# Kernel tuning notes

Measured on AMD Instinct MI355X. Metric: run time of the kernel, lower is better.

The kernel has to match this reference:

```python
import jax, jax.numpy as jnp
import numpy as np

N_NODES = 10000
N_EDGES = 320000
T = 24
H = 64


def setup_inputs() -> dict:
    key = jax.random.key(0)
    ks = jax.random.split(key, 16)
    s = 0.1  # keep LSTM gates in a sane range
    return {
        "blob": jax.random.normal(ks[0], (N_NODES, T), dtype=jnp.float32),
        "W_ih": s * jax.random.normal(ks[1], (N_NODES, 4 * H, 1), dtype=jnp.float32),
        "b_ih": s * jax.random.normal(ks[2], (N_NODES, 4 * H), dtype=jnp.float32),
        "W_hh": s * jax.random.normal(ks[3], (N_NODES, 4 * H, H), dtype=jnp.float32),
        "b_hh": s * jax.random.normal(ks[4], (N_NODES, 4 * H), dtype=jnp.float32),
        "Wg0": s * jax.random.normal(ks[5], (H, H), dtype=jnp.float32),
        "bg0": s * jax.random.normal(ks[6], (H,), dtype=jnp.float32),
        "Wg1": s * jax.random.normal(ks[7], (H, H), dtype=jnp.float32),
        "bg1": s * jax.random.normal(ks[8], (H,), dtype=jnp.float32),
        "Wg2": s * jax.random.normal(ks[9], (H, 1), dtype=jnp.float32),
        "bg2": s * jax.random.normal(ks[10], (1,), dtype=jnp.float32),
        "edge_src": jax.random.randint(ks[11], (N_EDGES,), 0, N_NODES, dtype=jnp.int32),
        "edge_dst": jax.random.randint(ks[12], (N_EDGES,), 0, N_NODES, dtype=jnp.int32),
    }


def _sym_norms(edge_src, edge_dst, n, dtype):
    ones = jnp.ones(edge_src.shape[0], dtype=dtype)
    deg_out = jax.ops.segment_sum(ones, edge_src, num_segments=n)
    deg_in = jax.ops.segment_sum(ones, edge_dst, num_segments=n)
    inv_sqrt = lambda d: jnp.where(d > 0, jnp.where(d > 0, d, 1.0) ** -0.5, 0.0)
    return inv_sqrt(deg_out), inv_sqrt(deg_in)


def reference(blob, W_ih, b_ih, W_hh, b_hh, Wg0, bg0, Wg1, bg1, Wg2, bg2,
              edge_src, edge_dst):
    n = blob.shape[0]
    norm_src, norm_dst = _sym_norms(edge_src, edge_dst, n, blob.dtype)

    def gconv(h, W, b, act=None):
        # DGL GraphConv, norm='both': D_dst^{-1/2} A D_src^{-1/2} h W + b
        msg = (h * norm_src[:, None])[edge_src]            # [E, F]
        agg = jax.ops.segment_sum(msg, edge_dst, num_segments=n)
        out = (agg * norm_dst[:, None]) @ W + b
        return act(out) if act is not None else out

    # Per-node LSTM, batched across all nodes; torch gate order i,f,g,o.
    Wx = W_ih[:, :, 0]  # [N, 4H] since in_feats == 1

    def step(carry, x_t):
        h, c = carry  # [N,H] each
        gates = (Wx * x_t[:, None] + b_ih
                 + jnp.einsum('nh,ngh->ng', h, W_hh) + b_hh)  # [N,4H]
        i, f, g, o = jnp.split(gates, 4, axis=1)
        c = jax.nn.sigmoid(f) * c + jax.nn.sigmoid(i) * jnp.tanh(g)
        h = jax.nn.sigmoid(o) * jnp.tanh(c)
        # GCN stack on current hidden states (dropout is identity at eval)
        z = gconv(h, Wg0, bg0, jax.nn.relu)
        z = gconv(z, Wg1, bg1, jax.nn.relu)
        z = gconv(z, Wg2, bg2)                               # [N,1]
        return (h, c), z[:, 0]

    h0 = jnp.zeros((n, H), dtype=blob.dtype)
    c0 = jnp.zeros((n, H), dtype=blob.dtype)
    _, ys = jax.lax.scan(step, (h0, c0), blob.T)  # ys: [T, N]
    return ys.T  # [N, T]
```

## Files before the change

### kernel.cpp

```cpp
#include <hip/hip_runtime.h>
#include <hip/hip_fp16.h>
#include <cstdint>
#include <cstddef>

#define NN 10000
#define NE 320000
#define TT 24
#define TP 12
#define HD 64
#define G4 256

__device__ __forceinline__ float sigm(float x){ return 1.0f/(1.0f + __expf(-x)); }
__device__ __forceinline__ float tanh_fast(float x){ return 2.0f/(1.0f + __expf(-2.0f*x)) - 1.0f; }

__global__ __launch_bounds__(256) void degree_kernel(const int* __restrict__ esrc, const int* __restrict__ edst,
                                                     int* __restrict__ deg_out, int* __restrict__ deg_in){
  int e = blockIdx.x*256 + threadIdx.x;
  if (e < NE){
    atomicAdd(&deg_out[esrc[e]], 1);
    atomicAdd(&deg_in[edst[e]], 1);
  }
}

__global__ __launch_bounds__(256) void norm_kernel(const int* __restrict__ deg_out, const int* __restrict__ deg_in,
                                                   float* __restrict__ norm_src, float* __restrict__ norm_dst){
  int i = blockIdx.x*256 + threadIdx.x;
  if (i < NN){
    int a = deg_out[i]; norm_src[i] = (a>0) ? rsqrtf((float)a) : 0.0f;
    int b = deg_in[i];  norm_dst[i] = (b>0) ? rsqrtf((float)b) : 0.0f;
  }
}

__global__ __launch_bounds__(256) void scan_kernel(const int* __restrict__ deg_in, int* __restrict__ csr_off,
                                                   int* __restrict__ cursor){
  __shared__ int sums[256];
  const int CH = (NN + 255)/256;
  int tid = threadIdx.x;
  int beg = tid*CH; if (beg > NN) beg = NN;
  int end = beg+CH; if (end > NN) end = NN;
  int s = 0;
  for (int i=beg;i<end;i++) s += deg_in[i];
  sums[tid] = s;
  __syncthreads();
  if (tid == 0){
    int run = 0;
    for (int i=0;i<256;i++){ int v = sums[i]; sums[i] = run; run += v; }
  }
  __syncthreads();
  int run = sums[tid];
  for (int i=beg;i<end;i++){ csr_off[i] = run; cursor[i] = run; run += deg_in[i]; }
  if (tid == 0) csr_off[NN] = NE;
}

__global__ __launch_bounds__(256) void fill_kernel(const int* __restrict__ esrc, const int* __restrict__ edst,
                                                   int* __restrict__ cursor, int2* __restrict__ csr_pk,
                                                   const float* __restrict__ norm_src){
  int e = blockIdx.x*256 + threadIdx.x;
  if (e < NE){
    int d = edst[e]; int s = esrc[e];
    int pos = atomicAdd(&cursor[d], 1);
    csr_pk[pos] = make_int2(s, __float_as_int(norm_src[s]));
  }
}

__global__ __launch_bounds__(256) void lstm_kernel(const float* __restrict__ blob, const float* __restrict__ W_ih,
                                                   const float* __restrict__ b_ih, const float* __restrict__ W_hh,
                                                   const float* __restrict__ b_hh, __half* __restrict__ h_all){
  const int n = blockIdx.x;
  const int g = threadIdx.x;
  __shared__ float lh[HD];
  __shared__ float lg[G4];

  float4 w4[16];
  const float4* wp = reinterpret_cast<const float4*>(W_hh + (size_t)n*(G4*HD) + (size_t)g*HD);
  #pragma unroll
  for (int i=0;i<16;i++) w4[i] = wp[i];

  const float wx = W_ih[(size_t)n*G4 + g];
  const float bs = b_ih[(size_t)n*G4 + g] + b_hh[(size_t)n*G4 + g];

  float c = 0.0f;
  if (g < HD) lh[g] = 0.0f;
  __syncthreads();

  for (int t=0;t<TT;t++){
    float xt = blob[n*TT + t];
    float gate = fmaf(wx, xt, bs);
    const float4* h4 = reinterpret_cast<const float4*>(lh);
    #pragma unroll
    for (int i=0;i<16;i++){
      float4 hv = h4[i];
      gate = fmaf(hv.x, w4[i].x, gate);
      gate = fmaf(hv.y, w4[i].y, gate);
      gate = fmaf(hv.z, w4[i].z, gate);
      gate = fmaf(hv.w, w4[i].w, gate);
    }
    lg[g] = gate;
    __syncthreads();
    if (g < HD){
      float iv = sigm(lg[g]);
      float fv = sigm(lg[HD+g]);
      float gv = tanh_fast(lg[2*HD+g]);
      float ov = sigm(lg[3*HD+g]);
      c = fmaf(fv, c, iv*gv);
      float h = ov * tanh_fast(c);
      lh[g] = h;
      h_all[(((size_t)n*TP + (t>>1))*HD + g)*2 + (t&1)] = __float2half(h);
    }
    __syncthreads();
  }
}

__global__ __launch_bounds__(256) void gconv_mid_kernel(const __half2* __restrict__ src_feat, __half2* __restrict__ dst_feat,
                                                        const float* __restrict__ Wg, const float* __restrict__ bg,
                                                        const int* __restrict__ csr_off, const int2* __restrict__ csr_pk,
                                                        const float* __restrict__ norm_dst){
  int wid = blockIdx.x*4 + (threadIdx.x >> 6);
  int lane = threadIdx.x & 63;
  if (wid >= NN*2) return;
  int n  = wid >> 1;
  int hf = wid & 1;
  const int tpo = hf*6;

  float wcol[HD];
  #pragma unroll
  for (int k=0;k<HD;k++) wcol[k] = Wg[k*HD + lane];
  float bias = bg[lane];

  float2 acc[6];
  #pragma unroll
  for (int j=0;j<6;j++) acc[j] = make_float2(0.f, 0.f);

  int e = csr_off[n];
  const int end = csr_off[n+1];
  for (; e+1 < end; e += 2){
    int2 p0 = csr_pk[e];
    int2 p1 = csr_pk[e+1];
    float w0 = __int_as_float(p0.y);
    float w1 = __int_as_float(p1.y);
    const __half2* b0 = src_feat + (size_t)p0.x*(TP*HD) + tpo*HD + lane;
    const __half2* b1 = src_feat + (size_t)p1.x*(TP*HD) + tpo*HD + lane;
    __half2 u0[6], u1[6];
    #pragma unroll
    for (int j=0;j<6;j++) u0[j] = b0[j*HD];
    #pragma unroll
    for (int j=0;j<6;j++) u1[j] = b1[j*HD];
    #pragma unroll
    for (int j=0;j<6;j++){
      float2 f0 = __half22float2(u0[j]);
      float2 f1 = __half22float2(u1[j]);
      acc[j].x = fmaf(w0, f0.x, acc[j].x);
      acc[j].y = fmaf(w0, f0.y, acc[j].y);
      acc[j].x = fmaf(w1, f1.x, acc[j].x);
      acc[j].y = fmaf(w1, f1.y, acc[j].y);
    }
  }
  if (e < end){
    int2 p0 = csr_pk[e];
    float w0 = __int_as_float(p0.y);
    const __half2* b0 = src_feat + (size_t)p0.x*(TP*HD) + tpo*HD + lane;
    #pragma unroll
    for (int j=0;j<6;j++){
      float2 f0 = __half22float2(b0[j*HD]);
      acc[j].x = fmaf(w0, f0.x, acc[j].x);
      acc[j].y = fmaf(w0, f0.y, acc[j].y);
    }
  }
  float nd = norm_dst[n];
  #pragma unroll
  for (int j=0;j<6;j++){ acc[j].x *= nd; acc[j].y *= nd; }

  __half2* dbase = dst_feat + (size_t)n*(TP*HD) + tpo*HD + lane;
  #pragma unroll
  for (int j=0;j<6;j++){
    float oe = bias, oo = bias;
    #pragma unroll
    for (int k=0;k<HD;k++){
      float ae = __shfl(acc[j].x, k, 64);
      float ao = __shfl(acc[j].y, k, 64);
      oe = fmaf(ae, wcol[k], oe);
      oo = fmaf(ao, wcol[k], oo);
    }
    oe = fmaxf(oe, 0.0f);
    oo = fmaxf(oo, 0.0f);
    dbase[j*HD] = __floats2half2_rn(oe, oo);
  }
}

__global__ __launch_bounds__(256) void gconv_last_kernel(const __half2* __restrict__ src_feat, float* __restrict__ q,
                                                         const float* __restrict__ Wg, const float* __restrict__ bg,
                                                         const float* __restrict__ Wg2,
                                                         const int* __restrict__ csr_off, const int2* __restrict__ csr_pk,
                                                         const float* __restrict__ norm_dst, const float* __restrict__ norm_src){
  int wid = blockIdx.x*4 + (threadIdx.x >> 6);
  int lane = threadIdx.x & 63;
  if (wid >= NN*2) return;
  int n  = wid >> 1;
  int hf = wid & 1;
  const int tpo = hf*6;

  float wcol[HD];
  #pragma unroll
  for (int k=0;k<HD;k++) wcol[k] = Wg[k*HD + lane];
  float bias = bg[lane];
  float w2 = Wg2[lane];

  float2 acc[6];
  #pragma unroll
  for (int j=0;j<6;j++) acc[j] = make_float2(0.f, 0.f);

  int e = csr_off[n];
  const int end = csr_off[n+1];
  for (; e+1 < end; e += 2){
    int2 p0 = csr_pk[e];
    int2 p1 = csr_pk[e+1];
    float w0 = __int_as_float(p0.y);
    float w1 = __int_as_float(p1.y);
    const __half2* b0 = src_feat + (size_t)p0.x*(TP*HD) + tpo*HD + lane;
    const __half2* b1 = src_feat + (size_t)p1.x*(TP*HD) + tpo*HD + lane;
    __half2 u0[6], u1[6];
    #pragma unroll
    for (int j=0;j<6;j++) u0[j] = b0[j*HD];
    #pragma unroll
    for (int j=0;j<6;j++) u1[j] = b1[j*HD];
    #pragma unroll
    for (int j=0;j<6;j++){
      float2 f0 = __half22float2(u0[j]);
      float2 f1 = __half22float2(u1[j]);
      acc[j].x = fmaf(w0, f0.x, acc[j].x);
      acc[j].y = fmaf(w0, f0.y, acc[j].y);
      acc[j].x = fmaf(w1, f1.x, acc[j].x);
      acc[j].y = fmaf(w1, f1.y, acc[j].y);
    }
  }
  if (e < end){
    int2 p0 = csr_pk[e];
    float w0 = __int_as_float(p0.y);
    const __half2* b0 = src_feat + (size_t)p0.x*(TP*HD) + tpo*HD + lane;
    #pragma unroll
    for (int j=0;j<6;j++){
      float2 f0 = __half22float2(b0[j*HD]);
      acc[j].x = fmaf(w0, f0.x, acc[j].x);
      acc[j].y = fmaf(w0, f0.y, acc[j].y);
    }
  }
  float nd = norm_dst[n];
  #pragma unroll
  for (int j=0;j<6;j++){ acc[j].x *= nd; acc[j].y *= nd; }

  float ns = norm_src[n];
  #pragma unroll
  for (int j=0;j<6;j++){
    float oe = bias, oo = bias;
    #pragma unroll
    for (int k=0;k<HD;k++){
      float ae = __shfl(acc[j].x, k, 64);
      float ao = __shfl(acc[j].y, k, 64);
      oe = fmaf(ae, wcol[k], oe);
      oo = fmaf(ao, wcol[k], oo);
    }
    oe = fmaxf(oe, 0.0f) * w2;
    oo = fmaxf(oo, 0.0f) * w2;
    #pragma unroll
    for (int off=32; off; off >>= 1){
      oe += __shfl_xor(oe, off, 64);
      oo += __shfl_xor(oo, off, 64);
    }
    if (lane == 0){
      int tp = tpo + j;
      q[n*32 + 2*tp]     = oe * ns;
      q[n*32 + 2*tp + 1] = oo * ns;
    }
  }
}

__global__ __launch_bounds__(256) void out_kernel(const float* __restrict__ q, const int* __restrict__ csr_off,
                                                  const int2* __restrict__ csr_pk, const float* __restrict__ norm_dst,
                                                  const float* __restrict__ bg2, float* __restrict__ out){
  int n = blockIdx.x*4 + (threadIdx.x >> 6);
  int lane = threadIdx.x & 63;
  if (n >= NN) return;
  int sub = lane >> 5;
  int tl  = lane & 31;
  bool act = tl < TT;
  int e = csr_off[n];
  const int end = csr_off[n+1];
  float s0 = 0.f, s1 = 0.f;
  for (; e+3 < end; e += 4){
    int a = csr_pk[e+sub].x;
    int b = csr_pk[e+2+sub].x;
    if (act){
      s0 += q[a*32 + tl];
      s1 += q[b*32 + tl];
    }
  }
  for (; e+1 < end; e += 2){
    int a = csr_pk[e+sub].x;
    if (act) s0 += q[a*32 + tl];
  }
  if (e < end && sub == 0 && act) s1 += q[csr_pk[e].x*32 + tl];
  float s = s0 + s1;
  s += __shfl_xor(s, 32, 64);
  if (sub == 0 && act) out[n*TT + tl] = fmaf(norm_dst[n], s, bg2[0]);
}

extern "C" void kernel_launch(void* const* d_in, const int* in_sizes, int n_in,
                              void* d_out, int out_size, void* d_ws, size_t ws_size,
                              hipStream_t stream) {
  (void)in_sizes; (void)n_in; (void)out_size; (void)ws_size;
  const float* blob  = (const float*)d_in[0];
  const float* W_ih  = (const float*)d_in[1];
  const float* b_ih  = (const float*)d_in[2];
  const float* W_hh  = (const float*)d_in[3];
  const float* b_hh  = (const float*)d_in[4];
  const float* Wg0   = (const float*)d_in[5];
  const float* bg0   = (const float*)d_in[6];
  const float* Wg1   = (const float*)d_in[7];
  const float* bg1   = (const float*)d_in[8];
  const float* Wg2   = (const float*)d_in[9];
  const float* bg2   = (const float*)d_in[10];
  const int* edge_src = (const int*)d_in[11];
  const int* edge_dst = (const int*)d_in[12];
  float* out = (float*)d_out;

  char* ws = (char*)d_ws;
  size_t off = 0;
  auto alloc = [&](size_t bytes)->char* {
    char* p = ws + off; off += (bytes + 255) & ~(size_t)255; return p;
  };
  __half* h_all   = (__half*)alloc((size_t)NN*TT*HD*sizeof(__half));
  __half* z1      = (__half*)alloc((size_t)NN*TT*HD*sizeof(__half));
  float*  q       = (float*) alloc((size_t)NN*32*sizeof(float));
  int*    deg_out = (int*)   alloc((size_t)NN*sizeof(int));
  int*    deg_in  = (int*)   alloc((size_t)NN*sizeof(int));
  float*  norm_src= (float*) alloc((size_t)NN*sizeof(float));
  float*  norm_dst= (float*) alloc((size_t)NN*sizeof(float));
  int*    csr_off = (int*)   alloc((size_t)(NN+1)*sizeof(int));
  int*    cursor  = (int*)   alloc((size_t)NN*sizeof(int));
  int2*   csr_pk  = (int2*)  alloc((size_t)NE*sizeof(int2));

  hipMemsetAsync(deg_out, 0, (size_t)NN*sizeof(int), stream);
  hipMemsetAsync(deg_in,  0, (size_t)NN*sizeof(int), stream);

  degree_kernel<<<(NE+255)/256, 256, 0, stream>>>(edge_src, edge_dst, deg_out, deg_in);
  norm_kernel<<<(NN+255)/256, 256, 0, stream>>>(deg_out, deg_in, norm_src, norm_dst);
  scan_kernel<<<1, 256, 0, stream>>>(deg_in, csr_off, cursor);
  fill_kernel<<<(NE+255)/256, 256, 0, stream>>>(edge_src, edge_dst, cursor, csr_pk, norm_src);

  lstm_kernel<<<NN, 256, 0, stream>>>(blob, W_ih, b_ih, W_hh, b_hh, h_all);

  gconv_mid_kernel<<<(NN*2+3)/4, 256, 0, stream>>>((const __half2*)h_all, (__half2*)z1, Wg0, bg0,
                                                   csr_off, csr_pk, norm_dst);
  gconv_last_kernel<<<(NN*2+3)/4, 256, 0, stream>>>((const __half2*)z1, q, Wg1, bg1, Wg2,
                                                    csr_off, csr_pk, norm_dst, norm_src);
  out_kernel<<<(NN+3)/4, 256, 0, stream>>>(q, csr_off, csr_pk, norm_dst, bg2, out);
}
```

Baseline: 1.406 ms.

## Store per-lane contiguous time features and stream GCN weights instead of register-caching

Changes the hidden-state layout so each feature lane's 12 half2 timestep pairs are contiguous per half, allowing 8-byte vector gathers per edge instead of six strided 4-byte loads. The LSTM buffers h in registers and writes it once at the end. The GCN kernels drop the 64-register weight column cache, load Wg per k inside a loop interchanged over time slots, and add an occupancy hint of 8 blocks. This aims to cut gather transactions and register pressure, at the cost of repeated weight loads from cache.

```diff
diff --git a/kernel.cpp b/kernel.cpp
--- a/kernel.cpp
+++ b/kernel.cpp
@@ -6,12 +6,21 @@
 #define NN 10000
 #define NE 320000
 #define TT 24
-#define TP 12
 #define HD 64
 #define G4 256
+#define NODE_HALFS (2*HD*12)
 
 __device__ __forceinline__ float sigm(float x){ return 1.0f/(1.0f + __expf(-x)); }
 __device__ __forceinline__ float tanh_fast(float x){ return 2.0f/(1.0f + __expf(-2.0f*x)) - 1.0f; }
+
+__device__ __forceinline__ float2 h2f2(unsigned int u){
+  __half2 h = *reinterpret_cast<const __half2*>(&u);
+  return __half22float2(h);
+}
+__device__ __forceinline__ unsigned int f2h2(float a, float b){
+  __half2 h = __floats2half2_rn(a, b);
+  return *reinterpret_cast<unsigned int*>(&h);
+}
 
 __global__ __launch_bounds__(256) void degree_kernel(const int* __restrict__ esrc, const int* __restrict__ edst,
                                                      int* __restrict__ deg_out, int* __restrict__ deg_in){
@@ -80,9 +89,12 @@
   const float bs = b_ih[(size_t)n*G4 + g] + b_hh[(size_t)n*G4 + g];
 
   float c = 0.0f;
+  float hprev = 0.0f;
+  unsigned int hb[12];
   if (g < HD) lh[g] = 0.0f;
   __syncthreads();
 
+  #pragma unroll
   for (int t=0;t<TT;t++){
     float xt = blob[n*TT + t];
     float gate = fmaf(wx, xt, bs);
@@ -105,13 +117,25 @@
       c = fmaf(fv, c, iv*gv);
       float h = ov * tanh_fast(c);
       lh[g] = h;
-      h_all[(((size_t)n*TP + (t>>1))*HD + g)*2 + (t&1)] = __float2half(h);
+      if (t & 1) hb[t>>1] = f2h2(hprev, h);
+      else       hprev = h;
     }
     __syncthreads();
   }
-}
-
-__global__ __launch_bounds__(256) void gconv_mid_kernel(const __half2* __restrict__ src_feat, __half2* __restrict__ dst_feat,
+  if (g < HD){
+    #pragma unroll
+    for (int hf=0; hf<2; hf++){
+      uint2* dst = reinterpret_cast<uint2*>(h_all + ((size_t)(n*2+hf)*HD + g)*12);
+      #pragma unroll
+      for (int m=0; m<3; m++){
+        uint2 s; s.x = hb[hf*6 + 2*m]; s.y = hb[hf*6 + 2*m + 1];
+        dst[m] = s;
+      }
+    }
+  }
+}
+
+__global__ __launch_bounds__(256, 8) void gconv_mid_kernel(const __half* __restrict__ src_feat, __half* __restrict__ dst_feat,
                                                         const float* __restrict__ Wg, const float* __restrict__ bg,
                                                         const int* __restrict__ csr_off, const int2* __restrict__ csr_pk,
                                                         const float* __restrict__ norm_dst){
@@ -120,12 +144,7 @@
   if (wid >= NN*2) return;
   int n  = wid >> 1;
   int hf = wid & 1;
-  const int tpo = hf*6;
-
-  float wcol[HD];
-  #pragma unroll
-  for (int k=0;k<HD;k++) wcol[k] = Wg[k*HD + lane];
-  float bias = bg[lane];
+  const size_t lane_off = ((size_t)hf*HD + lane)*12;
 
   float2 acc[6];
   #pragma unroll
@@ -138,56 +157,71 @@
     int2 p1 = csr_pk[e+1];
     float w0 = __int_as_float(p0.y);
     float w1 = __int_as_float(p1.y);
-    const __half2* b0 = src_feat + (size_t)p0.x*(TP*HD) + tpo*HD + lane;
-    const __half2* b1 = src_feat + (size_t)p1.x*(TP*HD) + tpo*HD + lane;
-    __half2 u0[6], u1[6];
-    #pragma unroll
-    for (int j=0;j<6;j++) u0[j] = b0[j*HD];
-    #pragma unroll
-    for (int j=0;j<6;j++) u1[j] = b1[j*HD];
-    #pragma unroll
-    for (int j=0;j<6;j++){
-      float2 f0 = __half22float2(u0[j]);
-      float2 f1 = __half22float2(u1[j]);
-      acc[j].x = fmaf(w0, f0.x, acc[j].x);
-      acc[j].y = fmaf(w0, f0.y, acc[j].y);
-      acc[j].x = fmaf(w1, f1.x, acc[j].x);
-      acc[j].y = fmaf(w1, f1.y, acc[j].y);
+    const uint2* b0 = reinterpret_cast<const uint2*>(src_feat + (size_t)p0.x*NODE_HALFS + lane_off);
+    const uint2* b1 = reinterpret_cast<const uint2*>(src_feat + (size_t)p1.x*NODE_HALFS + lane_off);
+    uint2 u0[3], u1[3];
+    #pragma unroll
+    for (int m=0;m<3;m++) u0[m] = b0[m];
+    #pragma unroll
+    for (int m=0;m<3;m++) u1[m] = b1[m];
+    #pragma unroll
+    for (int m=0;m<3;m++){
+      float2 f0a = h2f2(u0[m].x), f0b = h2f2(u0[m].y);
+      float2 f1a = h2f2(u1[m].x), f1b = h2f2(u1[m].y);
+      acc[2*m].x   = fmaf(w0, f0a.x, acc[2*m].x);
+      acc[2*m].y   = fmaf(w0, f0a.y, acc[2*m].y);
+      acc[2*m+1].x = fmaf(w0, f0b.x, acc[2*m+1].x);
+      acc[2*m+1].y = fmaf(w0, f0b.y, acc[2*m+1].y);
+      acc[2*m].x   = fmaf(w1, f1a.x, acc[2*m].x);
+      acc[2*m].y   = fmaf(w1, f1a.y, acc[2*m].y);
+      acc[2*m+1].x = fmaf(w1, f1b.x, acc[2*m+1].x);
+      acc[2*m+1].y = fmaf(w1, f1b.y, acc[2*m+1].y);
     }
   }
   if (e < end){
     int2 p0 = csr_pk[e];
     float w0 = __int_as_float(p0.y);
-    const __half2* b0 = src_feat + (size_t)p0.x*(TP*HD) + tpo*HD + lane;
+    const uint2* b0 = reinterpret_cast<const uint2*>(src_feat + (size_t)p0.x*NODE_HALFS + lane_off);
+    uint2 u0[3];
+    #pragma unroll
+    for (int m=0;m<3;m++) u0[m] = b0[m];
+    #pragma unroll
+    for (int m=0;m<3;m++){
+      float2 f0a = h2f2(u0[m].x), f0b = h2f2(u0[m].y);
+      acc[2*m].x   = fmaf(w0, f0a.x, acc[2*m].x);
+      acc[2*m].y   = fmaf(w0, f0a.y, acc[2*m].y);
+      acc[2*m+1].x = fmaf(w0, f0b.x, acc[2*m+1].x);
+      acc[2*m+1].y = fmaf(w0, f0b.y, acc[2*m+1].y);
+    }
+  }
+  float nd = norm_dst[n];
+  #pragma unroll
+  for (int j=0;j<6;j++){ acc[j].x *= nd; acc[j].y *= nd; }
+
+  float bias = bg[lane];
+  float oe[6], oo[6];
+  #pragma unroll
+  for (int j=0;j<6;j++){ oe[j] = bias; oo[j] = bias; }
+  #pragma unroll
+  for (int k=0;k<HD;k++){
+    float wk = Wg[k*HD + lane];
     #pragma unroll
     for (int j=0;j<6;j++){
-      float2 f0 = __half22float2(b0[j*HD]);
-      acc[j].x = fmaf(w0, f0.x, acc[j].x);
-      acc[j].y = fmaf(w0, f0.y, acc[j].y);
-    }
-  }
-  float nd = norm_dst[n];
-  #pragma unroll
-  for (int j=0;j<6;j++){ acc[j].x *= nd; acc[j].y *= nd; }
-
-  __half2* dbase = dst_feat + (size_t)n*(TP*HD) + tpo*HD + lane;
-  #pragma unroll
-  for (int j=0;j<6;j++){
-    float oe = bias, oo = bias;
-    #pragma unroll
-    for (int k=0;k<HD;k++){
-      float ae = __shfl(acc[j].x, k, 64);
-      float ao = __shfl(acc[j].y, k, 64);
-      oe = fmaf(ae, wcol[k], oe);
-      oo = fmaf(ao, wcol[k], oo);
-    }
-    oe = fmaxf(oe, 0.0f);
-    oo = fmaxf(oo, 0.0f);
-    dbase[j*HD] = __floats2half2_rn(oe, oo);
-  }
-}
-
-__global__ __launch_bounds__(256) void gconv_last_kernel(const __half2* __restrict__ src_feat, float* __restrict__ q,
+      oe[j] = fmaf(__shfl(acc[j].x, k, 64), wk, oe[j]);
+      oo[j] = fmaf(__shfl(acc[j].y, k, 64), wk, oo[j]);
+    }
+  }
+  uint2* dst = reinterpret_cast<uint2*>(dst_feat + (size_t)n*NODE_HALFS + lane_off);
+  #pragma unroll
+  for (int m=0;m<3;m++){
+    uint2 s;
+    s.x = f2h2(fmaxf(oe[2*m],   0.0f), fmaxf(oo[2*m],   0.0f));
+    s.y = f2h2(fmaxf(oe[2*m+1], 0.0f), fmaxf(oo[2*m+1], 0.0f));
+    dst[m] = s;
+  }
+}
+
+__global__ __launch_bounds__(256, 8) void gconv_last_kernel(const __half* __restrict__ src_feat, float* __restrict__ q,
                                                          const float* __restrict__ Wg, const float* __restrict__ bg,
                                                          const float* __restrict__ Wg2,
                                                          const int* __restrict__ csr_off, const int2* __restrict__ csr_pk,
@@ -197,13 +231,7 @@
   if (wid >= NN*2) return;
   int n  = wid >> 1;
   int hf = wid & 1;
-  const int tpo = hf*6;
-
-  float wcol[HD];
-  #pragma unroll
-  for (int k=0;k<HD;k++) wcol[k] = Wg[k*HD + lane];
-  float bias = bg[lane];
-  float w2 = Wg2[lane];
+  const size_t lane_off = ((size_t)hf*HD + lane)*12;
 
   float2 acc[6];
   #pragma unroll
@@ -216,60 +244,74 @@
     int2 p1 = csr_pk[e+1];
     float w0 = __int_as_float(p0.y);
     float w1 = __int_as_float(p1.y);
-    const __half2* b0 = src_feat + (size_t)p0.x*(TP*HD) + tpo*HD + lane;
-    const __half2* b1 = src_feat + (size_t)p1.x*(TP*HD) + tpo*HD + lane;
-    __half2 u0[6], u1[6];
-    #pragma unroll
-    for (int j=0;j<6;j++) u0[j] = b0[j*HD];
-    #pragma unroll
-    for (int j=0;j<6;j++) u1[j] = b1[j*HD];
-    #pragma unroll
-    for (int j=0;j<6;j++){
-      float2 f0 = __half22float2(u0[j]);
-      float2 f1 = __half22float2(u1[j]);
-      acc[j].x = fmaf(w0, f0.x, acc[j].x);
-      acc[j].y = fmaf(w0, f0.y, acc[j].y);
-      acc[j].x = fmaf(w1, f1.x, acc[j].x);
-      acc[j].y = fmaf(w1, f1.y, acc[j].y);
+    const uint2* b0 = reinterpret_cast<const uint2*>(src_feat + (size_t)p0.x*NODE_HALFS + lane_off);
+    const uint2* b1 = reinterpret_cast<const uint2*>(src_feat + (size_t)p1.x*NODE_HALFS + lane_off);
+    uint2 u0[3], u1[3];
+    #pragma unroll
+    for (int m=0;m<3;m++) u0[m] = b0[m];
+    #pragma unroll
+    for (int m=0;m<3;m++) u1[m] = b1[m];
+    #pragma unroll
+    for (int m=0;m<3;m++){
+      float2 f0a = h2f2(u0[m].x), f0b = h2f2(u0[m].y);
+      float2 f1a = h2f2(u1[m].x), f1b = h2f2(u1[m].y);
+      acc[2*m].x   = fmaf(w0, f0a.x, acc[2*m].x);
+      acc[2*m].y   = fmaf(w0, f0a.y, acc[2*m].y);
+      acc[2*m+1].x = fmaf(w0, f0b.x, acc[2*m+1].x);
+      acc[2*m+1].y = fmaf(w0, f0b.y, acc[2*m+1].y);
+      acc[2*m].x   = fmaf(w1, f1a.x, acc[2*m].x);
+      acc[2*m].y   = fmaf(w1, f1a.y, acc[2*m].y);
+      acc[2*m+1].x = fmaf(w1, f1b.x, acc[2*m+1].x);
+      acc[2*m+1].y = fmaf(w1, f1b.y, acc[2*m+1].y);
     }
   }
   if (e < end){
     int2 p0 = csr_pk[e];
     float w0 = __int_as_float(p0.y);
-    const __half2* b0 = src_feat + (size_t)p0.x*(TP*HD) + tpo*HD + lane;
+    const uint2* b0 = reinterpret_cast<const uint2*>(src_feat + (size_t)p0.x*NODE_HALFS + lane_off);
+    uint2 u0[3];
+    #pragma unroll
+    for (int m=0;m<3;m++) u0[m] = b0[m];
+    #pragma unroll
+    for (int m=0;m<3;m++){
+      float2 f0a = h2f2(u0[m].x), f0b = h2f2(u0[m].y);
+      acc[2*m].x   = fmaf(w0, f0a.x, acc[2*m].x);
+      acc[2*m].y   = fmaf(w0, f0a.y, acc[2*m].y);
+      acc[2*m+1].x = fmaf(w0, f0b.x, acc[2*m+1].x);
+      acc[2*m+1].y = fmaf(w0, f0b.y, acc[2*m+1].y);
+    }
+  }
+  float nd = norm_dst[n];
+  #pragma unroll
+  for (int j=0;j<6;j++){ acc[j].x *= nd; acc[j].y *= nd; }
+
+  float bias = bg[lane];
+  float w2v = Wg2[lane];
+  float oe[6], oo[6];
+  #pragma unroll
+  for (int j=0;j<6;j++){ oe[j] = bias; oo[j] = bias; }
+  #pragma unroll
+  for (int k=0;k<HD;k++){
+    float wk = Wg[k*HD + lane];
     #pragma unroll
     for (int j=0;j<6;j++){
-      float2 f0 = __half22float2(b0[j*HD]);
-      acc[j].x = fmaf(w0, f0.x, acc[j].x);
-      acc[j].y = fmaf(w0, f0.y, acc[j].y);
-    }
-  }
-  float nd = norm_dst[n];
-  #pragma unroll
-  for (int j=0;j<6;j++){ acc[j].x *= nd; acc[j].y *= nd; }
-
+      oe[j] = fmaf(__shfl(acc[j].x, k, 64), wk, oe[j]);
+      oo[j] = fmaf(__shfl(acc[j].y, k, 64), wk, oo[j]);
+    }
+  }
   float ns = norm_src[n];
   #pragma unroll
   for (int j=0;j<6;j++){
-    float oe = bias, oo = bias;
-    #pragma unroll
-    for (int k=0;k<HD;k++){
-      float ae = __shfl(acc[j].x, k, 64);
-      float ao = __shfl(acc[j].y, k, 64);
-      oe = fmaf(ae, wcol[k], oe);
-      oo = fmaf(ao, wcol[k], oo);
-    }
-    oe = fmaxf(oe, 0.0f) * w2;
-    oo = fmaxf(oo, 0.0f) * w2;
+    float se = fmaxf(oe[j], 0.0f) * w2v;
+    float so = fmaxf(oo[j], 0.0f) * w2v;
     #pragma unroll
     for (int off=32; off; off >>= 1){
-      oe += __shfl_xor(oe, off, 64);
-      oo += __shfl_xor(oo, off, 64);
+      se += __shfl_xor(se, off, 64);
+      so += __shfl_xor(so, off, 64);
     }
     if (lane == 0){
-      int tp = tpo + j;
-      q[n*32 + 2*tp]     = oe * ns;
-      q[n*32 + 2*tp + 1] = oo * ns;
+      q[n*32 + hf*12 + 2*j]     = se * ns;
+      q[n*32 + hf*12 + 2*j + 1] = so * ns;
     }
   }
 }
@@ -349,9 +391,7 @@
 
   lstm_kernel<<<NN, 256, 0, stream>>>(blob, W_ih, b_ih, W_hh, b_hh, h_all);
 
-  gconv_mid_kernel<<<(NN*2+3)/4, 256, 0, stream>>>((const __half2*)h_all, (__half2*)z1, Wg0, bg0,
-                                                   csr_off, csr_pk, norm_dst);
-  gconv_last_kernel<<<(NN*2+3)/4, 256, 0, stream>>>((const __half2*)z1, q, Wg1, bg1, Wg2,
-                                                    csr_off, csr_pk, norm_dst, norm_src);
+  gconv_mid_kernel<<<(NN*2)/4, 256, 0, stream>>>(h_all, z1, Wg0, bg0, csr_off, csr_pk, norm_dst);
+  gconv_last_kernel<<<(NN*2)/4, 256, 0, stream>>>(z1, q, Wg1, bg1, Wg2, csr_off, csr_pk, norm_dst, norm_src);
   out_kernel<<<(NN+3)/4, 256, 0, stream>>>(q, csr_off, csr_pk, norm_dst, bg2, out);
 }
```

New measurement: 3.104 ms. 121% more time.
